# Kernel tuning notes

Measured on AMD Instinct MI355X. Metric: run time of the kernel, lower is better.

## Reference

```python
import jax, jax.numpy as jnp
import numpy as np

B, N, E = 2, 50000, 800000
IN_CH, SP_CH, OUT_CH, EDGE_CH = 64, 16, 32, 1


def _xavier(k, shape):
    scale = (2.0 / (shape[0] + shape[1])) ** 0.5
    return jax.random.normal(k, shape, dtype=jnp.float32) * scale


def setup_inputs() -> dict:
    key = jax.random.key(0)
    ks = jax.random.split(key, 20)
    return {
        "X": jax.random.normal(ks[0], (B, N, IN_CH), dtype=jnp.float32),
        "edge_index0": jax.random.randint(ks[1], (2, E), 0, N),
        "edge_index1": jax.random.randint(ks[2], (2, E), 0, N),
        "edge_weight0": jax.random.uniform(ks[3], (E, EDGE_CH), dtype=jnp.float32),
        "edge_weight1": jax.random.uniform(ks[4], (E, EDGE_CH), dtype=jnp.float32),
        "res_n_id0": jnp.arange(N),
        "res_n_id1": jnp.arange(N),
        # conv1 params (in=IN_CH, out=SP_CH)
        "value1": _xavier(ks[5], (IN_CH, SP_CH)),
        "key1": _xavier(ks[6], (SP_CH, SP_CH)),
        "query1": _xavier(ks[7], (SP_CH, SP_CH)),
        "we1": _xavier(ks[8], (EDGE_CH, SP_CH)),
        "att_w1": _xavier(ks[9], (3 * SP_CH, 1)),
        "att_b1": jnp.zeros((1,), jnp.float32),
        "cat_w1": _xavier(ks[10], (2 * SP_CH, SP_CH)),
        "cat_b1": jnp.zeros((SP_CH,), jnp.float32),
        # conv2 params (in=SP_CH, out=OUT_CH)
        "value2": _xavier(ks[11], (SP_CH, OUT_CH)),
        "key2": _xavier(ks[12], (OUT_CH, OUT_CH)),
        "query2": _xavier(ks[13], (OUT_CH, OUT_CH)),
        "we2": _xavier(ks[14], (EDGE_CH, OUT_CH)),
        "att_w2": _xavier(ks[15], (3 * OUT_CH, 1)),
        "att_b2": jnp.zeros((1,), jnp.float32),
        "cat_w2": _xavier(ks[16], (2 * OUT_CH, OUT_CH)),
        "cat_b2": jnp.zeros((OUT_CH,), jnp.float32),
    }


def _egnn_conv(Xs, Xd, ei, ef, value, key_w, query_w, we, att_w, att_b, cat_w, cat_b):
    # Xs: [B,Ns,Cin] source nodes, Xd: [B,Nd,Cin] dest nodes, ei: [2,E], ef: [E,edge_ch]
    xs = Xs @ value                       # [B,Ns,C]
    xd = Xd @ value                       # [B,Nd,C]
    e = ef @ we                           # [E,C]
    xj = xs[:, ei[0]]                     # [B,E,C] source gather
    xi = xd[:, ei[1]]                     # [B,E,C] dest gather
    q = xj @ query_w                      # note: original code names are swapped; kept faithful
    k = xi @ key_w
    att_in = jnp.concatenate([k, q, jnp.broadcast_to(e, q.shape)], axis=-1)  # [B,E,3C]
    att = jax.nn.sigmoid(att_in @ att_w + att_b)      # [B,E,1]
    msg = att * xj * jax.nn.sigmoid(e)                # [B,E,C]
    aggr = jnp.zeros(xd.shape, xd.dtype).at[:, ei[1]].add(msg)  # scatter-add over dest
    upd = jnp.concatenate([xd, aggr], axis=-1) @ cat_w + cat_b  # [B,Nd,C]
    return xd + jax.nn.relu(upd)


def reference(X, edge_index0, edge_index1, edge_weight0, edge_weight1,
              res_n_id0, res_n_id1,
              value1, key1, query1, we1, att_w1, att_b1, cat_w1, cat_b1,
              value2, key2, query2, we2, att_w2, att_b2, cat_w2, cat_b2):
    X1 = _egnn_conv(X, X[:, res_n_id0], edge_index0, edge_weight0,
                    value1, key1, query1, we1, att_w1, att_b1, cat_w1, cat_b1)
    X1 = jax.nn.leaky_relu(X1)  # negative_slope 0.01, matches torch default
    X2 = _egnn_conv(X1, X1[:, res_n_id1], edge_index1, edge_weight1,
                    value2, key2, query2, we2, att_w2, att_b2, cat_w2, cat_b2)
    return X2
```

## Files before the change

kernel.cpp:

```cpp
#include <hip/hip_runtime.h>
#include <hip/hip_fp16.h>

#define BB   2
#define NN   50000
#define EE   800000
#define INCH 64
#define C1   16
#define C2   32
#define NB   (BB*NN)

#define W1S   6
#define W2S   5
#define NBK1  ((NN + 63) >> 6)
#define NBK2  ((NN + 31) >> 5)
#define NBKT  (NBK1 + NBK2)
#define EB    4096
#define TPB   1024
#define NEBLK ((2*EE + EB - 1) / EB)

#define OFF_XS1   0
#define OFF_XS2   (OFF_XS1 + NB*C1/2)
#define OFF_DOTK1 (OFF_XS2 + NB*C2/2)
#define OFF_DOTQ1 (OFF_DOTK1 + NB)
#define OFF_DOTK2 (OFF_DOTQ1 + NB)
#define OFF_DOTQ2 (OFF_DOTK2 + NB)
#define OFF_AG1   (OFF_DOTQ2 + NB)
#define OFF_AG2   (OFF_AG1 + NN*32)
#define OFF_BTOT  (OFF_AG2 + NN*64)
#define OFF_BBASE (OFF_BTOT + NBKT)
#define OFF_START (OFF_BBASE + NBKT)
#define OFF_DEG   (OFF_START + 2*NN)
#define OFF_SC    (OFF_DEG + 2*NN)
#define OFF_RECS2 (OFF_SC + 2)
#define OFF_REGION (OFF_RECS2 + 2*EE*2)
#define OFF_RECS   OFF_REGION
#define OFF_BCNT   (OFF_REGION + 2*EE*2)
#define OFF_PREC   OFF_REGION

__device__ __forceinline__ float sigmoidf(float x) {
    return __builtin_amdgcn_rcpf(1.0f + __expf(-x));
}

__device__ __forceinline__ float h2f_u(unsigned u) {
    return __half2float(__ushort_as_half((unsigned short)u));
}

__global__ __launch_bounds__(TPB) void k_value1cnt(
        const float* __restrict__ X, const float* __restrict__ value1,
        const float* __restrict__ key1, const float* __restrict__ query1,
        const float* __restrict__ aw1,
        const int* __restrict__ ei0, const int* __restrict__ ei1,
        const float* __restrict__ we1, const float* __restrict__ we2,
        const float* __restrict__ aw2,
        __half* __restrict__ xs1h, float* __restrict__ dotk1,
        float* __restrict__ dotq1, unsigned* __restrict__ blockCnt,
        float* __restrict__ sc) {
    __shared__ float W[INCH*C1];
    __shared__ float KV[C1], QV[C1];
    __shared__ unsigned h[NBKT];
    int tid = threadIdx.x;
    if (tid < 256) {
        for (int i = tid; i < INCH*C1; i += 256) W[i] = value1[i];
        if (tid < C1) {
            float kv = 0.f, qv = 0.f;
#pragma unroll
            for (int j = 0; j < C1; ++j) {
                kv += key1[tid*C1+j]   * aw1[j];
                qv += query1[tid*C1+j] * aw1[C1+j];
            }
            KV[tid] = kv; QV[tid] = qv;
        }
    } else {
        for (int i = tid - 256; i < NBKT; i += 768) h[i] = 0u;
        if (blockIdx.x == 0 && tid == 256) {
            float e = 0.f;
            for (int j = 0; j < C1; ++j) e += we1[j] * aw1[2*C1+j];
            sc[0] = e;
        }
        if (blockIdx.x == 0 && tid == 257) {
            float e = 0.f;
            for (int j = 0; j < C2; ++j) e += we2[j] * aw2[2*C2+j];
            sc[1] = e;
        }
    }
    __syncthreads();
    if (tid < 256) {
        int bn = blockIdx.x * 256 + tid;
        if (bn < NB) {
            int b = (bn >= NN) ? 1 : 0;
            int node = bn - b*NN;
            const float4* Xr = (const float4*)(X + (size_t)bn * INCH);
            float acc[C1];
#pragma unroll
            for (int j = 0; j < C1; ++j) acc[j] = 0.f;
#pragma unroll
            for (int v = 0; v < 16; ++v) {
                float4 p = Xr[v];
                float x4[4] = {p.x, p.y, p.z, p.w};
#pragma unroll
                for (int hh = 0; hh < 4; ++hh) {
                    int i = v*4 + hh;
                    float xv = x4[hh];
#pragma unroll
                    for (int j = 0; j < C1; ++j) acc[j] += xv * W[i*C1+j];
                }
            }
            float dk = 0.f, dq = 0.f;
#pragma unroll
            for (int j = 0; j < C1; ++j) { dk += acc[j]*KV[j]; dq += acc[j]*QV[j]; }
            __half* o = xs1h + ((size_t)node * C1) * 2 + b;
#pragma unroll
            for (int j = 0; j < C1; ++j) o[2*j] = __float2half_rn(acc[j]);
            dotk1[node*2 + b] = dk; dotq1[node*2 + b] = dq;
        }
    } else {
        int base = blockIdx.x * EB;
        for (int j = tid - 256; j < EB; j += 768) {
            int t = base + j;
            if (t < 2*EE) {
                int bkt;
                if (t < EE) { int dst = ei0[EE + t];      bkt = dst >> W1S; }
                else        { int dst = ei1[EE + t - EE]; bkt = NBK1 + (dst >> W2S); }
                atomicAdd(&h[bkt], 1u);
            }
        }
    }
    __syncthreads();
    unsigned* o = blockCnt + (size_t)blockIdx.x * NBKT;
    for (int i = tid; i < NBKT; i += TPB) o[i] = h[i];
}

__global__ __launch_bounds__(512) void k_scanBkt(
        unsigned* __restrict__ blockCnt, unsigned* __restrict__ bktTot) {
    __shared__ unsigned s[512];
    int tid = threadIdx.x;
    int bkt = blockIdx.x;
    unsigned v = (tid < NEBLK) ? blockCnt[(size_t)tid * NBKT + bkt] : 0u;
    s[tid] = v;
    __syncthreads();
    for (int o = 1; o < 512; o <<= 1) {
        unsigned t = (tid >= o) ? s[tid - o] : 0u;
        __syncthreads();
        s[tid] += t;
        __syncthreads();
    }
    if (tid < NEBLK) blockCnt[(size_t)tid * NBKT + bkt] = s[tid] - v;
    if (tid == 511) bktTot[bkt] = s[511];
}

__global__ __launch_bounds__(1024) void k_scanTot(
        const unsigned* __restrict__ bktTot, unsigned* __restrict__ bucketBase) {
    __shared__ unsigned s[1024];
    int tid = threadIdx.x;
    int base = tid * 3;
    unsigned a0 = (base + 0 < NBKT) ? bktTot[base + 0] : 0u;
    unsigned a1 = (base + 1 < NBKT) ? bktTot[base + 1] : 0u;
    unsigned a2 = (base + 2 < NBKT) ? bktTot[base + 2] : 0u;
    unsigned l = a0 + a1 + a2;
    s[tid] = l;
    __syncthreads();
    for (int o = 1; o < 1024; o <<= 1) {
        unsigned t = (tid >= o) ? s[tid - o] : 0u;
        __syncthreads();
        s[tid] += t;
        __syncthreads();
    }
    unsigned ex = s[tid] - l;
    if (base + 0 < NBKT) bucketBase[base + 0] = ex;
    if (base + 1 < NBKT) bucketBase[base + 1] = ex + a0;
    if (base + 2 < NBKT) bucketBase[base + 2] = ex + a0 + a1;
}

__global__ __launch_bounds__(TPB) void k_permute(
        const int* __restrict__ ei0, const int* __restrict__ ei1,
        const float* __restrict__ ew0, const float* __restrict__ ew1,
        const unsigned* __restrict__ blockOff, const unsigned* __restrict__ bucketBase,
        uint2* __restrict__ recs) {
    __shared__ unsigned off[NBKT];
    __shared__ unsigned cur[NBKT];
    int tid = threadIdx.x;
    const unsigned* bo = blockOff + (size_t)blockIdx.x * NBKT;
    for (int i = tid; i < NBKT; i += TPB) { off[i] = bo[i] + bucketBase[i]; cur[i] = 0u; }
    __syncthreads();
    int base = blockIdx.x * EB;
#pragma unroll
    for (int j = 0; j < EB/TPB; ++j) {
        int t = base + j*TPB + tid;
        if (t >= 2*EE) break;
        int bkt, dl, src; float ef;
        if (t < EE) {
            int dst = ei0[EE + t];
            bkt = dst >> W1S; dl = dst & 63;
            src = ei0[t]; ef = ew0[t];
        } else {
            int e = t - EE;
            int dst = ei1[EE + e];
            bkt = NBK1 + (dst >> W2S); dl = dst & 31;
            src = ei1[e]; ef = ew1[e];
        }
        unsigned pos = off[bkt] + atomicAdd(&cur[bkt], 1u);
        recs[pos] = make_uint2((unsigned)src | ((unsigned)dl << 16), __float_as_uint(ef));
    }
}

__global__ __launch_bounds__(256) void k_sortbp(
        const uint2* __restrict__ recs, const unsigned* __restrict__ bktTot,
        const unsigned* __restrict__ bucketBase,
        const float* __restrict__ dotk1, const float* __restrict__ dotq1,
        const float* __restrict__ ab1, const float* __restrict__ sc,
        uint2* __restrict__ recs2, unsigned* __restrict__ startA,
        unsigned* __restrict__ degA) {
    __shared__ unsigned h[64], sOff[64], cur[64];
    int tid = threadIdx.x;
    int bkt = blockIdx.x;
    int lay1 = (bkt < NBK1) ? 1 : 0;
    int ndl  = lay1 ? 64 : 32;
    int nodeBase = lay1 ? (bkt << W1S) : ((bkt - NBK1) << W2S);
    int layOff   = lay1 ? 0 : NN;
    if (tid < 64) h[tid] = 0u;
    __syncthreads();
    unsigned cnt = bktTot[bkt], base = bucketBase[bkt];
    for (unsigned i = tid; i < cnt; i += 256)
        atomicAdd(&h[recs[base + i].x >> 16], 1u);
    __syncthreads();
    if (tid == 0) {
        unsigned run = 0;
        for (int d = 0; d < ndl; ++d) { sOff[d] = run; run += h[d]; }
    }
    __syncthreads();
    if (tid < ndl) {
        cur[tid] = sOff[tid];
        int node = nodeBase + tid;
        if (node < NN) {
            startA[layOff + node] = base + sOff[tid];
            degA[layOff + node]   = h[tid];
        }
    }
    __syncthreads();
    float ec = sc[0], ab0 = ab1[0];
    for (unsigned i = tid; i < cnt; i += 256) {
        uint2 r = recs[base + i];
        unsigned dl  = r.x >> 16;
        unsigned src = r.x & 0xffffu;
        unsigned pos = atomicAdd(&cur[dl], 1u);
        unsigned dst = (unsigned)nodeBase + dl;
        if (lay1) {
            float ef = __uint_as_float(r.y);
            float eb = ef * ec + ab0;
            float2 dk = *(const float2*)(dotk1 + dst*2);
            float2 dq = *(const float2*)(dotq1 + src*2);
            float p0 = sigmoidf(dk.x + dq.x + eb);
            float p1 = sigmoidf(dk.y + dq.y + eb);
            unsigned pu = __builtin_bit_cast(unsigned, __floats2half2_rn(p0, p1));
            unsigned eu = (unsigned)__half_as_ushort(__float2half_rn(ef));
            recs2[base + pos] = make_uint2(src | (pu << 16),
                                           (pu >> 16) | (eu << 16));
        } else {
            recs2[base + pos] = make_uint2(src | (dst << 16), r.y);
        }
    }
}

__global__ __launch_bounds__(256) void k_prep(
        const uint2* __restrict__ recs2seg, const float* __restrict__ dotk,
        const float* __restrict__ dotq, const float* __restrict__ ab,
        const float* __restrict__ sc, int scIdx, uint2* __restrict__ prec) {
    int e = blockIdx.x * 256 + threadIdx.x;
    uint2 r = recs2seg[e];
    int src = r.x & 0xffff, dst = r.x >> 16;
    float ef = __uint_as_float(r.y);
    float eb = ef * sc[scIdx] + ab[0];
    float2 dk = *(const float2*)(dotk + dst*2);
    float2 dq = *(const float2*)(dotq + src*2);
    float p0 = sigmoidf(dk.x + dq.x + eb);
    float p1 = sigmoidf(dk.y + dq.y + eb);
    unsigned pu = __builtin_bit_cast(unsigned, __floats2half2_rn(p0, p1));
    unsigned eu = (unsigned)__half_as_ushort(__float2half_rn(ef));
    prec[e] = make_uint2((unsigned)src | (pu << 16),
                         (pu >> 16) | (eu << 16));
}

__global__ __launch_bounds__(256) void k_aggr1f(
        const uint2* __restrict__ prec, const float* __restrict__ we,
        const uint2* __restrict__ xsh,
        const unsigned* __restrict__ startA, const unsigned* __restrict__ degA,
        float* __restrict__ aggrf) {
    int t = blockIdx.x * 256 + threadIdx.x;
    int node = t >> 4, sub = t & 15, cp = sub & 7, h = sub >> 3;
    unsigned s = startA[node];
    unsigned n = degA[node];
    float w0 = we[2*cp], w1 = we[2*cp+1];
    float a0 = 0.f, a1 = 0.f, a2 = 0.f, a3 = 0.f;
    unsigned i = (unsigned)h;
    uint2 r_n = make_uint2(0u, 0u); uint2 xr_n = make_uint2(0u, 0u);
    if (i < n) {
        r_n  = prec[s + i];
        xr_n = xsh[(size_t)(r_n.x & 0xffff)*8 + cp];
    }
    for (; i < n; i += 2) {
        uint2 r = r_n; uint2 xr = xr_n;
        if (i + 2 < n) {
            r_n  = prec[s + i + 2];
            xr_n = xsh[(size_t)(r_n.x & 0xffff)*8 + cp];
        }
        float p0 = h2f_u(r.x >> 16);
        float p1 = h2f_u(r.y & 0xffff);
        float ef = h2f_u(r.y >> 16);
        float se0 = sigmoidf(ef * w0);
        float se1 = sigmoidf(ef * w1);
        float2 f0 = __half22float2(__builtin_bit_cast(__half2, xr.x));
        float2 f1 = __half22float2(__builtin_bit_cast(__half2, xr.y));
        a0 += p0 * se0 * f0.x;
        a1 += p1 * se0 * f0.y;
        a2 += p0 * se1 * f1.x;
        a3 += p1 * se1 * f1.y;
    }
    a0 += __shfl_xor(a0, 8); a1 += __shfl_xor(a1, 8);
    a2 += __shfl_xor(a2, 8); a3 += __shfl_xor(a3, 8);
    if (h == 0)
        ((float4*)aggrf)[(size_t)node*8 + cp] = make_float4(a0, a1, a2, a3);
}

__global__ __launch_bounds__(256) void k_update1(
        const float* __restrict__ cat_w, const float* __restrict__ cat_b,
        const float* __restrict__ value2,
        const float* __restrict__ key2, const float* __restrict__ query2,
        const float* __restrict__ aw2,
        const __half* __restrict__ xs1h, const float* __restrict__ aggr1f,
        __half* __restrict__ xs2h, float* __restrict__ dotk2, float* __restrict__ dotq2) {
    __shared__ float CW[2*C1*C1];
    __shared__ float CB[C1];
    __shared__ float V2[C1*C2];
    __shared__ float KV[C2], QV[C2];
    int tid = threadIdx.x;
    for (int i = tid; i < 2*C1*C1; i += 256) CW[i] = cat_w[i];
    for (int i = tid; i < C1*C2;   i += 256) V2[i] = value2[i];
    if (tid < C1) CB[tid] = cat_b[tid];
    if (tid < C2) {
        float kv = 0.f;
#pragma unroll
        for (int j = 0; j < C2; ++j) kv += key2[tid*C2+j] * aw2[j];
        KV[tid] = kv;
    } else if (tid < 2*C2) {
        int c = tid - C2;
        float qv = 0.f;
#pragma unroll
        for (int j = 0; j < C2; ++j) qv += query2[c*C2+j] * aw2[C2+j];
        QV[c] = qv;
    }
    __syncthreads();
    int bn = blockIdx.x * 256 + tid;
    if (bn >= NB) return;
    int b = (bn >= NN) ? 1 : 0;
    int node = bn - b*NN;
    int bs = b * 16;
    float xd[C1], ag[C1];
    {
        const uint4* xv = (const uint4*)(xs1h + (size_t)node * C1 * 2);
#pragma unroll
        for (int v = 0; v < 4; ++v) {
            uint4 q = xv[v];
            xd[4*v+0] = h2f_u(q.x >> bs);
            xd[4*v+1] = h2f_u(q.y >> bs);
            xd[4*v+2] = h2f_u(q.z >> bs);
            xd[4*v+3] = h2f_u(q.w >> bs);
        }
    }
    {
        const float4* av = (const float4*)(aggr1f + (size_t)node * 32);
#pragma unroll
        for (int w = 0; w < 8; ++w) {
            float4 f = av[w];
            ag[2*w]   = b ? f.y : f.x;
            ag[2*w+1] = b ? f.w : f.z;
        }
    }
    float x1[C1];
#pragma unroll
    for (int j = 0; j < C1; ++j) {
        float u = CB[j];
#pragma unroll
        for (int i = 0; i < C1; ++i) {
            u += xd[i] * CW[i*C1 + j];
            u += ag[i] * CW[(C1+i)*C1 + j];
        }
        float o = xd[j] + fmaxf(u, 0.f);
        x1[j] = (o > 0.f) ? o : 0.01f * o;
    }
    float o2[C2];
#pragma unroll
    for (int k = 0; k < C2; ++k) o2[k] = 0.f;
#pragma unroll
    for (int j = 0; j < C1; ++j) {
        float xv = x1[j];
#pragma unroll
        for (int k = 0; k < C2; ++k) o2[k] += xv * V2[j*C2 + k];
    }
    float dk = 0.f, dq = 0.f;
#pragma unroll
    for (int k = 0; k < C2; ++k) { dk += o2[k]*KV[k]; dq += o2[k]*QV[k]; }
    __half* o = xs2h + ((size_t)node*C2)*2 + b;
#pragma unroll
    for (int k = 0; k < C2; ++k) o[2*k] = __float2half_rn(o2[k]);
    dotk2[node*2 + b] = dk; dotq2[node*2 + b] = dq;
}

__global__ __launch_bounds__(256) void k_aggr2u(
        const uint2* __restrict__ prec, const float* __restrict__ we,
        const uint2* __restrict__ xsh,
        const unsigned* __restrict__ startA, const unsigned* __restrict__ degA,
        const float* __restrict__ cat_w, const float* __restrict__ cat_b,
        const __half* __restrict__ xs2h, float* __restrict__ out) {
    __shared__ float CW[2*C2*C2];
    __shared__ float CB[C2];
    __shared__ float agS[8*64];
    __shared__ float xdS[8*2*32];
    int tid = threadIdx.x;
    for (int i = tid; i < 2*C2*C2; i += 256) CW[i] = cat_w[i];
    if (tid < C2) CB[tid] = cat_b[tid];

    int nl = tid >> 5, sub = tid & 31, cp = sub & 15, h = sub >> 4;
    int node = blockIdx.x * 8 + nl;
    unsigned s = startA[NN + node] - EE;
    unsigned n = degA[NN + node];
    float w0 = we[2*cp], w1 = we[2*cp+1];
    float a0 = 0.f, a1 = 0.f, a2 = 0.f, a3 = 0.f;
    unsigned i = (unsigned)h;
    uint2 r_n = make_uint2(0u, 0u); uint2 xr_n = make_uint2(0u, 0u);
    if (i < n) {
        r_n  = prec[s + i];
        xr_n = xsh[(size_t)(r_n.x & 0xffff)*16 + cp];
    }
    for (; i < n; i += 2) {
        uint2 r = r_n; uint2 xr = xr_n;
        if (i + 2 < n) {
            r_n  = prec[s + i + 2];
            xr_n = xsh[(size_t)(r_n.x & 0xffff)*16 + cp];
        }
        float p0 = h2f_u(r.x >> 16);
        float p1 = h2f_u(r.y & 0xffff);
        float ef = h2f_u(r.y >> 16);
        float se0 = sigmoidf(ef * w0);
        float se1 = sigmoidf(ef * w1);
        float2 f0 = __half22float2(__builtin_bit_cast(__half2, xr.x));
        float2 f1 = __half22float2(__builtin_bit_cast(__half2, xr.y));
        a0 += p0 * se0 * f0.x;
        a1 += p1 * se0 * f0.y;
        a2 += p0 * se1 * f1.x;
        a3 += p1 * se1 * f1.y;
    }
    a0 += __shfl_xor(a0, 16); a1 += __shfl_xor(a1, 16);
    a2 += __shfl_xor(a2, 16); a3 += __shfl_xor(a3, 16);
    if (h == 0)
        ((float4*)agS)[nl*16 + cp] = make_float4(a0, a1, a2, a3);

    {
        unsigned w = ((const unsigned*)(xs2h))[(size_t)(blockIdx.x*8) * 32 + tid];
        int snl = tid >> 5, sc_ = tid & 31;
        xdS[(snl*2 + 0)*32 + sc_] = h2f_u(w);
        xdS[(snl*2 + 1)*32 + sc_] = h2f_u(w >> 16);
    }
    __syncthreads();

    int b  = (tid >> 4) & 1;
    int kk = tid & 15;
    const float* xdp = &xdS[(nl*2 + b)*32];
    const float* agp = &agS[nl*64];
    float u0 = CB[kk], u1 = CB[kk+16];
#pragma unroll
    for (int ii = 0; ii < C2; ++ii) {
        float xv = xdp[ii];
        float av = agp[(ii>>1)*4 + (ii&1)*2 + b];
        u0 += xv * CW[ii*C2 + kk]        + av * CW[(C2+ii)*C2 + kk];
        u1 += xv * CW[ii*C2 + kk + 16]   + av * CW[(C2+ii)*C2 + kk + 16];
    }
    float o0 = xdp[kk]    + fmaxf(u0, 0.f);
    float o1 = xdp[kk+16] + fmaxf(u1, 0.f);
    float* orow = out + ((size_t)(b*NN + node)) * C2;
    orow[kk]      = o0;
    orow[kk + 16] = o1;
}

extern "C" void kernel_launch(void* const* d_in, const int* in_sizes, int n_in,
                              void* d_out, int out_size, void* d_ws, size_t ws_size,
                              hipStream_t stream) {
    const float* X      = (const float*)d_in[0];
    const int*   ei0    = (const int*)d_in[1];
    const int*   ei1    = (const int*)d_in[2];
    const float* ew0    = (const float*)d_in[3];
    const float* ew1    = (const float*)d_in[4];
    const float* value1 = (const float*)d_in[7];
    const float* key1   = (const float*)d_in[8];
    const float* query1 = (const float*)d_in[9];
    const float* we1    = (const float*)d_in[10];
    const float* aw1    = (const float*)d_in[11];
    const float* ab1    = (const float*)d_in[12];
    const float* cw1    = (const float*)d_in[13];
    const float* cb1    = (const float*)d_in[14];
    const float* value2 = (const float*)d_in[15];
    const float* key2   = (const float*)d_in[16];
    const float* query2 = (const float*)d_in[17];
    const float* we2    = (const float*)d_in[18];
    const float* aw2    = (const float*)d_in[19];
    const float* ab2    = (const float*)d_in[20];
    const float* cw2    = (const float*)d_in[21];
    const float* cb2    = (const float*)d_in[22];
    float* ws  = (float*)d_ws;
    float* out = (float*)d_out;

    __half* xs1h = (__half*)(ws + OFF_XS1);
    __half* xs2h = (__half*)(ws + OFF_XS2);
    float* aggr1f = ws + OFF_AG1;
    unsigned* blockCnt   = (unsigned*)(ws + OFF_BCNT);
    unsigned* bktTot     = (unsigned*)(ws + OFF_BTOT);
    unsigned* bucketBase = (unsigned*)(ws + OFF_BBASE);
    unsigned* startA     = (unsigned*)(ws + OFF_START);
    unsigned* degA       = (unsigned*)(ws + OFF_DEG);
    uint2*    recs2      = (uint2*)(ws + OFF_RECS2);
    uint2*    recs       = (uint2*)(ws + OFF_RECS);
    uint2*    prec2      = (uint2*)(ws + OFF_PREC);

    k_value1cnt<<<NEBLK, TPB, 0, stream>>>(X, value1, key1, query1, aw1,
                                           ei0, ei1, we1, we2, aw2,
                                           xs1h, ws + OFF_DOTK1, ws + OFF_DOTQ1,
                                           blockCnt, ws + OFF_SC);

    k_scanBkt<<<NBKT, 512, 0, stream>>>(blockCnt, bktTot);
    k_scanTot<<<1, 1024, 0, stream>>>(bktTot, bucketBase);
    k_permute<<<NEBLK, TPB, 0, stream>>>(ei0, ei1, ew0, ew1,
                                         blockCnt, bucketBase, recs);
    k_sortbp<<<NBKT, 256, 0, stream>>>(recs, bktTot, bucketBase,
                                       ws + OFF_DOTK1, ws + OFF_DOTQ1,
                                       ab1, ws + OFF_SC,
                                       recs2, startA, degA);

    k_aggr1f<<<(NN*16)/256, 256, 0, stream>>>(recs2, we1, (const uint2*)xs1h,
                                              startA, degA, aggr1f);
    k_update1<<<(NB+255)/256, 256, 0, stream>>>(cw1, cb1, value2, key2, query2, aw2,
                                                xs1h, aggr1f,
                                                xs2h, ws + OFF_DOTK2, ws + OFF_DOTQ2);

    k_prep<<<EE/256, 256, 0, stream>>>(recs2 + EE, ws + OFF_DOTK2, ws + OFF_DOTQ2,
                                       ab2, ws + OFF_SC, 1, prec2);
    k_aggr2u<<<NN/8, 256, 0, stream>>>(prec2, we2, (const uint2*)xs2h,
                                       startA, degA, cw2, cb2, xs2h, out);
}
```

Before: 292.9 us.

## Fuse layer-1 aggregation with node update and pad shared arrays

Merges the layer-1 edge aggregation kernel with the per-node update kernel, so the aggregate stays in shared memory and is no longer written to and re-read from a global buffer. Each block now handles 16 nodes and splits the cat_w, value2 and key/query dot-product work across threads, using shuffle reductions. Shared arrays in both fused kernels are padded to reduce bank conflicts. The cost is extra shared memory and barriers per block, plus the weight-loading prologue running in every aggregation block.

```diff
diff --git a/kernel.cpp b/kernel.cpp
--- a/kernel.cpp
+++ b/kernel.cpp
@@ -280,13 +280,42 @@
                          (pu >> 16) | (eu << 16));
 }
 
-__global__ __launch_bounds__(256) void k_aggr1f(
+__global__ __launch_bounds__(256) void k_aggr1u(
         const uint2* __restrict__ prec, const float* __restrict__ we,
         const uint2* __restrict__ xsh,
         const unsigned* __restrict__ startA, const unsigned* __restrict__ degA,
-        float* __restrict__ aggrf) {
-    int t = blockIdx.x * 256 + threadIdx.x;
-    int node = t >> 4, sub = t & 15, cp = sub & 7, h = sub >> 3;
+        const float* __restrict__ cat_w, const float* __restrict__ cat_b,
+        const float* __restrict__ value2,
+        const float* __restrict__ key2, const float* __restrict__ query2,
+        const float* __restrict__ aw2, const __half* __restrict__ xs1h,
+        __half* __restrict__ xs2h, float* __restrict__ dotk2,
+        float* __restrict__ dotq2) {
+    __shared__ float CW[2*C1*C1];
+    __shared__ float CB[C1];
+    __shared__ float V2[C1*C2];
+    __shared__ float KV[C2], QV[C2];
+    __shared__ float agS[16*36];
+    __shared__ float xdS[16*2*17];
+    __shared__ float x1S[16*2*17];
+    int tid = threadIdx.x;
+    for (int i = tid; i < 2*C1*C1; i += 256) CW[i] = cat_w[i];
+    for (int i = tid; i < C1*C2;   i += 256) V2[i] = value2[i];
+    if (tid < C1) CB[tid] = cat_b[tid];
+    if (tid < C2) {
+        float kv = 0.f;
+#pragma unroll
+        for (int j = 0; j < C2; ++j) kv += key2[tid*C2+j] * aw2[j];
+        KV[tid] = kv;
+    } else if (tid < 2*C2) {
+        int c = tid - C2;
+        float qv = 0.f;
+#pragma unroll
+        for (int j = 0; j < C2; ++j) qv += query2[c*C2+j] * aw2[C2+j];
+        QV[c] = qv;
+    }
+
+    int nl = tid >> 4, sub = tid & 15, cp = sub & 7, h = sub >> 3;
+    int node = blockIdx.x * 16 + nl;
     unsigned s = startA[node];
     unsigned n = degA[node];
     float w0 = we[2*cp], w1 = we[2*cp+1];
@@ -318,91 +347,55 @@
     a0 += __shfl_xor(a0, 8); a1 += __shfl_xor(a1, 8);
     a2 += __shfl_xor(a2, 8); a3 += __shfl_xor(a3, 8);
     if (h == 0)
-        ((float4*)aggrf)[(size_t)node*8 + cp] = make_float4(a0, a1, a2, a3);
-}
-
-__global__ __launch_bounds__(256) void k_update1(
-        const float* __restrict__ cat_w, const float* __restrict__ cat_b,
-        const float* __restrict__ value2,
-        const float* __restrict__ key2, const float* __restrict__ query2,
-        const float* __restrict__ aw2,
-        const __half* __restrict__ xs1h, const float* __restrict__ aggr1f,
-        __half* __restrict__ xs2h, float* __restrict__ dotk2, float* __restrict__ dotq2) {
-    __shared__ float CW[2*C1*C1];
-    __shared__ float CB[C1];
-    __shared__ float V2[C1*C2];
-    __shared__ float KV[C2], QV[C2];
-    int tid = threadIdx.x;
-    for (int i = tid; i < 2*C1*C1; i += 256) CW[i] = cat_w[i];
-    for (int i = tid; i < C1*C2;   i += 256) V2[i] = value2[i];
-    if (tid < C1) CB[tid] = cat_b[tid];
-    if (tid < C2) {
-        float kv = 0.f;
-#pragma unroll
-        for (int j = 0; j < C2; ++j) kv += key2[tid*C2+j] * aw2[j];
-        KV[tid] = kv;
-    } else if (tid < 2*C2) {
-        int c = tid - C2;
-        float qv = 0.f;
-#pragma unroll
-        for (int j = 0; j < C2; ++j) qv += query2[c*C2+j] * aw2[C2+j];
-        QV[c] = qv;
-    }
-    __syncthreads();
-    int bn = blockIdx.x * 256 + tid;
-    if (bn >= NB) return;
-    int b = (bn >= NN) ? 1 : 0;
-    int node = bn - b*NN;
-    int bs = b * 16;
-    float xd[C1], ag[C1];
+        ((float4*)(agS + nl*36))[cp] = make_float4(a0, a1, a2, a3);
+
     {
-        const uint4* xv = (const uint4*)(xs1h + (size_t)node * C1 * 2);
-#pragma unroll
-        for (int v = 0; v < 4; ++v) {
-            uint4 q = xv[v];
-            xd[4*v+0] = h2f_u(q.x >> bs);
-            xd[4*v+1] = h2f_u(q.y >> bs);
-            xd[4*v+2] = h2f_u(q.z >> bs);
-            xd[4*v+3] = h2f_u(q.w >> bs);
-        }
-    }
+        unsigned w = ((const unsigned*)(xs1h))[(size_t)(blockIdx.x*16) * 16 + tid];
+        int snl = tid >> 4, sc_ = tid & 15;
+        xdS[(snl*2 + 0)*17 + sc_] = h2f_u(w);
+        xdS[(snl*2 + 1)*17 + sc_] = h2f_u(w >> 16);
+    }
+    __syncthreads();
+
+    int b  = (tid >> 3) & 1;
+    int kk = tid & 7;
+    const float* xdp = &xdS[(nl*2 + b)*17];
+    const float* agp = &agS[nl*36];
     {
-        const float4* av = (const float4*)(aggr1f + (size_t)node * 32);
-#pragma unroll
-        for (int w = 0; w < 8; ++w) {
-            float4 f = av[w];
-            ag[2*w]   = b ? f.y : f.x;
-            ag[2*w+1] = b ? f.w : f.z;
-        }
-    }
-    float x1[C1];
-#pragma unroll
-    for (int j = 0; j < C1; ++j) {
-        float u = CB[j];
-#pragma unroll
-        for (int i = 0; i < C1; ++i) {
-            u += xd[i] * CW[i*C1 + j];
-            u += ag[i] * CW[(C1+i)*C1 + j];
-        }
-        float o = xd[j] + fmaxf(u, 0.f);
-        x1[j] = (o > 0.f) ? o : 0.01f * o;
-    }
-    float o2[C2];
-#pragma unroll
-    for (int k = 0; k < C2; ++k) o2[k] = 0.f;
-#pragma unroll
-    for (int j = 0; j < C1; ++j) {
-        float xv = x1[j];
-#pragma unroll
-        for (int k = 0; k < C2; ++k) o2[k] += xv * V2[j*C2 + k];
-    }
-    float dk = 0.f, dq = 0.f;
-#pragma unroll
-    for (int k = 0; k < C2; ++k) { dk += o2[k]*KV[k]; dq += o2[k]*QV[k]; }
-    __half* o = xs2h + ((size_t)node*C2)*2 + b;
-#pragma unroll
-    for (int k = 0; k < C2; ++k) o[2*k] = __float2half_rn(o2[k]);
-    dotk2[node*2 + b] = dk; dotq2[node*2 + b] = dq;
+        int j0 = kk, j1 = kk + 8;
+        float u0 = CB[j0], u1 = CB[j1];
+#pragma unroll
+        for (int i2 = 0; i2 < C1; ++i2) {
+            float xv = xdp[i2];
+            float av = agp[(i2>>1)*4 + (i2&1)*2 + b];
+            u0 += xv * CW[i2*C1 + j0] + av * CW[(C1+i2)*C1 + j0];
+            u1 += xv * CW[i2*C1 + j1] + av * CW[(C1+i2)*C1 + j1];
+        }
+        float o0 = xdp[j0] + fmaxf(u0, 0.f);
+        float o1 = xdp[j1] + fmaxf(u1, 0.f);
+        float* x1p = &x1S[(nl*2 + b)*17];
+        x1p[j0] = (o0 > 0.f) ? o0 : 0.01f * o0;
+        x1p[j1] = (o1 > 0.f) ? o1 : 0.01f * o1;
+    }
+    __syncthreads();
+    {
+        const float* x1p = &x1S[(nl*2 + b)*17];
+        float dk = 0.f, dq = 0.f;
+        __half* orow = xs2h + (size_t)node * C2 * 2 + b;
+#pragma unroll
+        for (int kq = 0; kq < 4; ++kq) {
+            int k = kk + kq*8;
+            float o2 = 0.f;
+#pragma unroll
+            for (int j = 0; j < C1; ++j) o2 += x1p[j] * V2[j*C2 + k];
+            orow[2*k] = __float2half_rn(o2);
+            dk += o2 * KV[k]; dq += o2 * QV[k];
+        }
+        dk += __shfl_xor(dk, 1); dq += __shfl_xor(dq, 1);
+        dk += __shfl_xor(dk, 2); dq += __shfl_xor(dq, 2);
+        dk += __shfl_xor(dk, 4); dq += __shfl_xor(dq, 4);
+        if (kk == 0) { dotk2[node*2 + b] = dk; dotq2[node*2 + b] = dq; }
+    }
 }
 
 __global__ __launch_bounds__(256) void k_aggr2u(
@@ -413,8 +406,8 @@
         const __half* __restrict__ xs2h, float* __restrict__ out) {
     __shared__ float CW[2*C2*C2];
     __shared__ float CB[C2];
-    __shared__ float agS[8*64];
-    __shared__ float xdS[8*2*32];
+    __shared__ float agS[8*68];
+    __shared__ float xdS[8*2*33];
     int tid = threadIdx.x;
     for (int i = tid; i < 2*C2*C2; i += 256) CW[i] = cat_w[i];
     if (tid < C2) CB[tid] = cat_b[tid];
@@ -452,20 +445,20 @@
     a0 += __shfl_xor(a0, 16); a1 += __shfl_xor(a1, 16);
     a2 += __shfl_xor(a2, 16); a3 += __shfl_xor(a3, 16);
     if (h == 0)
-        ((float4*)agS)[nl*16 + cp] = make_float4(a0, a1, a2, a3);
+        ((float4*)(agS + nl*68))[cp] = make_float4(a0, a1, a2, a3);
 
     {
         unsigned w = ((const unsigned*)(xs2h))[(size_t)(blockIdx.x*8) * 32 + tid];
         int snl = tid >> 5, sc_ = tid & 31;
-        xdS[(snl*2 + 0)*32 + sc_] = h2f_u(w);
-        xdS[(snl*2 + 1)*32 + sc_] = h2f_u(w >> 16);
+        xdS[(snl*2 + 0)*33 + sc_] = h2f_u(w);
+        xdS[(snl*2 + 1)*33 + sc_] = h2f_u(w >> 16);
     }
     __syncthreads();
 
     int b  = (tid >> 4) & 1;
     int kk = tid & 15;
-    const float* xdp = &xdS[(nl*2 + b)*32];
-    const float* agp = &agS[nl*64];
+    const float* xdp = &xdS[(nl*2 + b)*33];
+    const float* agp = &agS[nl*68];
     float u0 = CB[kk], u1 = CB[kk+16];
 #pragma unroll
     for (int ii = 0; ii < C2; ++ii) {
@@ -510,7 +503,6 @@
 
     __half* xs1h = (__half*)(ws + OFF_XS1);
     __half* xs2h = (__half*)(ws + OFF_XS2);
-    float* aggr1f = ws + OFF_AG1;
     unsigned* blockCnt   = (unsigned*)(ws + OFF_BCNT);
     unsigned* bktTot     = (unsigned*)(ws + OFF_BTOT);
     unsigned* bucketBase = (unsigned*)(ws + OFF_BBASE);
@@ -534,11 +526,10 @@
                                        ab1, ws + OFF_SC,
                                        recs2, startA, degA);
 
-    k_aggr1f<<<(NN*16)/256, 256, 0, stream>>>(recs2, we1, (const uint2*)xs1h,
-                                              startA, degA, aggr1f);
-    k_update1<<<(NB+255)/256, 256, 0, stream>>>(cw1, cb1, value2, key2, query2, aw2,
-                                                xs1h, aggr1f,
-                                                xs2h, ws + OFF_DOTK2, ws + OFF_DOTQ2);
+    k_aggr1u<<<NN/16, 256, 0, stream>>>(recs2, we1, (const uint2*)xs1h,
+                                        startA, degA, cw1, cb1,
+                                        value2, key2, query2, aw2, xs1h,
+                                        xs2h, ws + OFF_DOTK2, ws + OFF_DOTQ2);
 
     k_prep<<<EE/256, 256, 0, stream>>>(recs2 + EE, ws + OFF_DOTK2, ws + OFF_DOTQ2,
                                        ab2, ws + OFF_SC, 1, prec2);
```

New measurement: 289.5 us. About the same (-1.2%).
